# Performance work log

Measured on AMD Instinct MI355X. Metric: run time of the kernel, lower is better.

Reference implementation:

```python
import jax, jax.numpy as jnp
import numpy as np

# SLAYER neuron/simulation constants (netParams)
THETA = 10.0      # spike threshold
TAU_SR = 10.0     # PSP (SRM alpha) time constant
TAU_REF = 1.0     # refractory time constant
TAU_RHO = 1.0     # surrogate-gradient width
SCALE_RHO = 1.0   # surrogate-gradient scale
TS = 1.0          # simulation timestep
K_EPS = 100       # truncated FIR length of the alpha PSP kernel
REF_DECAY = float(np.exp(-TS / TAU_REF))


@jax.custom_vjp
def _spike_fn(v):
    # heaviside threshold with SLAYER-style exponential surrogate gradient
    return (v >= 0.0).astype(v.dtype)

def _spike_fwd(v):
    return (v >= 0.0).astype(v.dtype), v

def _spike_bwd(v, g):
    return (g * (SCALE_RHO / TAU_RHO) * jnp.exp(-jnp.abs(v) / TAU_RHO),)

_spike_fn.defvjp(_spike_fwd, _spike_bwd)


def psp(x):
    """Causal temporal filter with SRM alpha kernel eps(t)=(t/tau)exp(1-t/tau)."""
    shp = x.shape
    T = shp[-1]
    t = jnp.arange(K_EPS, dtype=x.dtype) * TS
    eps = (t / TAU_SR) * jnp.exp(1.0 - t / TAU_SR)
    xr = x.reshape(-1, 1, T)  # [N,1,T]
    y = jax.lax.conv_general_dilated(xr, eps[::-1].reshape(1, 1, K_EPS), (1,), [(K_EPS - 1, 0)])
    return y.reshape(shp)


def spike(u):
    """Sequential threshold with decaying refractory state (scan over time)."""
    uT = jnp.moveaxis(u, -1, 0)  # [T, ...]

    def step(r, u_t):
        s = _spike_fn(u_t + r - THETA)
        return REF_DECAY * r - 2.0 * THETA * s, s

    _, sT = jax.lax.scan(step, jnp.zeros(uT.shape[1:], uT.dtype), uT)
    return jnp.moveaxis(sT, 0, -1)


def pool(x, k):
    # SLAYER pool: fixed-weight sum conv, weight = 1.1*theta/(k*k) per element
    B, C, H, W, T = x.shape
    return x.reshape(B, C, H // k, k, W // k, k, T).sum(axis=(3, 5)) * (1.1 * THETA / (k * k))


def conv(x, w, pad):
    # 3D conv with time-pointwise kernel == per-timestep 2D conv (fold T into batch)
    B, C, H, W, T = x.shape
    xr = jnp.moveaxis(x, -1, 1).reshape(B * T, C, H, W)
    y = jax.lax.conv_general_dilated(xr, w, (1, 1), [(pad, pad), (pad, pad)])
    return jnp.moveaxis(y.reshape(B, T, w.shape[0], H, W), 1, -1)


def delay(x, d):
    """Per-channel learnable temporal delay via linear interpolation gather."""
    T = x.shape[-1]
    C = d.shape[0]
    t = jnp.arange(T, dtype=x.dtype)
    src = t[None, :] - d[:, None]            # [C, T]
    i0 = jnp.floor(src)
    w = (src - i0).reshape((1, C, 1, 1, T))
    i0 = i0.astype(jnp.int32)

    def take(idx):
        v = jnp.take_along_axis(x, jnp.clip(idx, 0, T - 1).reshape((1, C, 1, 1, T)), axis=-1)
        ok = ((idx >= 0) & (idx < T)).reshape((1, C, 1, 1, T))
        return jnp.where(ok, v, 0.0)

    return take(i0) * (1.0 - w) + take(i0 + 1) * w


def setup_inputs() -> dict:
    key = jax.random.key(0)
    ks = jax.random.split(key, 9)
    B, T = 4, 300
    spikeInput = (jax.random.uniform(ks[0], (B, 2, 128, 128, T)) < 0.03).astype(jnp.float32)
    conv1_w = jax.random.normal(ks[1], (16, 2, 5, 5), jnp.float32) * (1.0 / np.sqrt(2 * 25))
    conv2_w = jax.random.normal(ks[2], (32, 16, 3, 3), jnp.float32) * (1.0 / np.sqrt(16 * 9))
    fc1_w = jax.random.normal(ks[3], (512, 2048), jnp.float32) * (1.0 / np.sqrt(2048))
    fc2_w = jax.random.normal(ks[4], (11, 512), jnp.float32) * (1.0 / np.sqrt(512))
    delay1_d = jax.random.uniform(ks[5], (16,), jnp.float32) * 4.0
    delay2_d = jax.random.uniform(ks[6], (32,), jnp.float32) * 4.0
    delay3_d = jax.random.uniform(ks[7], (512,), jnp.float32) * 4.0
    return {"spikeInput": spikeInput, "conv1_w": conv1_w, "conv2_w": conv2_w,
            "fc1_w": fc1_w, "fc2_w": fc2_w,
            "delay1_d": delay1_d, "delay2_d": delay2_d, "delay3_d": delay3_d}


def reference(spikeInput, conv1_w, conv2_w, fc1_w, fc2_w, delay1_d, delay2_d, delay3_d):
    s = spike(pool(psp(spikeInput), 4))          # [B,2,32,32,T]
    s = spike(conv(psp(s), conv1_w, 2))          # [B,16,32,32,T]
    s = delay(s, delay1_d)
    s = spike(pool(psp(s), 2))                   # [B,16,16,16,T]
    s = spike(conv(psp(s), conv2_w, 1))          # [B,32,16,16,T]
    s = delay(s, delay2_d)
    s = spike(pool(psp(s), 2))                   # [B,32,8,8,T]
    B, C, H, W, T = s.shape
    s = s.reshape(B, C * H * W, 1, 1, T)         # [B,2048,1,1,T]
    s = spike(jnp.einsum('oi,bixyt->boxyt', fc1_w, psp(s)))  # [B,512,1,1,T]
    s = delay(s, delay3_d)
    s = spike(jnp.einsum('oi,bixyt->boxyt', fc2_w, psp(s)))  # [B,11,1,1,T]
    return s
```

## Files before the change

kernel.cpp:

```cpp
#include <hip/hip_runtime.h>

#define TLEN 300
#define THETA 10.0f
#define REF_DECAY 0.36787944117144233f

__global__ void eps_init_kernel(float* __restrict__ eps) {
  int k = threadIdx.x;
  if (k < 104) eps[k] = 0.f;
  if (k < 100) {
    float a = (float)k / 10.0f;
    eps[k] = a * expf(1.0f - a);
  }
}

#define FIRSTEP(e, A, B, C)                                                              \
  acc[0] += e.x * B.x; acc[1] += e.x * B.y; acc[2] += e.x * B.z; acc[3] += e.x * B.w;    \
  acc[4] += e.x * C.x; acc[5] += e.x * C.y; acc[6] += e.x * C.z; acc[7] += e.x * C.w;    \
  acc[0] += e.y * A.w; acc[1] += e.y * B.x; acc[2] += e.y * B.y; acc[3] += e.y * B.z;    \
  acc[4] += e.y * B.w; acc[5] += e.y * C.x; acc[6] += e.y * C.y; acc[7] += e.y * C.z;    \
  acc[0] += e.z * A.z; acc[1] += e.z * A.w; acc[2] += e.z * B.x; acc[3] += e.z * B.y;    \
  acc[4] += e.z * B.z; acc[5] += e.z * B.w; acc[6] += e.z * C.x; acc[7] += e.z * C.y;    \
  acc[0] += e.w * A.y; acc[1] += e.w * A.z; acc[2] += e.w * A.w; acc[3] += e.w * B.x;    \
  acc[4] += e.w * B.y; acc[5] += e.w * B.z; acc[6] += e.w * B.w; acc[7] += e.w * C.x;

__device__ __forceinline__ float4 ldq(const float* __restrict__ rowp, int w) {
  if (w >= 0 && w < TLEN) return *reinterpret_cast<const float4*>(rowp + w);
  return make_float4(0.f, 0.f, 0.f, 0.f);
}

__global__ __launch_bounds__(256) void fir_direct_kernel(const float* __restrict__ in,
                                                         float* __restrict__ out,
                                                         const float* __restrict__ epsg,
                                                         int rows) {
  int task = blockIdx.x * 256 + threadIdx.x;
  int row = task / 38;
  int l = task - row * 38;
  if (row >= rows) return;
  const float* rowp = in + (long)row * TLEN;
  const int t0 = 8 * l;
  float4 A = ldq(rowp, t0 - 4);
  float4 B = ldq(rowp, t0);
  float4 C = ldq(rowp, t0 + 4);
  float acc[8];
#pragma unroll
  for (int j = 0; j < 8; ++j) acc[j] = 0.f;
#pragma unroll 1
  for (int kg0 = 0; kg0 < 80; kg0 += 20) {
    const float* ep = epsg + kg0;
#pragma unroll
    for (int kk = 0; kk < 5; ++kk) {
      const float4 e = *reinterpret_cast<const float4*>(ep + 4 * kk);
      const int kg = kg0 + 4 * kk;
      FIRSTEP(e, A, B, C);
      C = B; B = A;
      A = ldq(rowp, t0 - kg - 8);
    }
    __builtin_amdgcn_sched_barrier(0);
  }
#pragma unroll
  for (int kk = 0; kk < 5; ++kk) {
    const float4 e = *reinterpret_cast<const float4*>(epsg + 80 + 4 * kk);
    FIRSTEP(e, A, B, C);
    C = B; B = A;
    if (kk < 4) A = ldq(rowp, t0 - 88 - 4 * kk);
  }
  float* op = out + (long)row * TLEN + t0;
  *reinterpret_cast<float4*>(op) = make_float4(acc[0], acc[1], acc[2], acc[3]);
  if (t0 + 4 < TLEN)
    *reinterpret_cast<float4*>(op + 4) = make_float4(acc[4], acc[5], acc[6], acc[7]);
}

__global__ __launch_bounds__(64) void scan_kernel(float* __restrict__ u, long rows) {
  long row = (long)blockIdx.x * 64 + threadIdx.x;
  if (row >= rows) return;
  float* p = u + row * TLEN;
  float4 q0 = *reinterpret_cast<const float4*>(p);
  float4 q1 = *reinterpret_cast<const float4*>(p + 4);
  float4 q2 = *reinterpret_cast<const float4*>(p + 8);
  float4 q3 = *reinterpret_cast<const float4*>(p + 12);
  float ref = 0.f;
#pragma unroll 4
  for (int c4 = 0; c4 < 75; ++c4) {
    float4 u4 = q0;
    q0 = q1; q1 = q2; q2 = q3;
    if (c4 < 71) q3 = *reinterpret_cast<const float4*>(p + 4 * (c4 + 4));
    float v, sp;
    v = u4.x + ref - THETA; sp = (v >= 0.f) ? 1.f : 0.f; u4.x = sp; ref = REF_DECAY * ref - 20.0f * sp;
    v = u4.y + ref - THETA; sp = (v >= 0.f) ? 1.f : 0.f; u4.y = sp; ref = REF_DECAY * ref - 20.0f * sp;
    v = u4.z + ref - THETA; sp = (v >= 0.f) ? 1.f : 0.f; u4.z = sp; ref = REF_DECAY * ref - 20.0f * sp;
    v = u4.w + ref - THETA; sp = (v >= 0.f) ? 1.f : 0.f; u4.w = sp; ref = REF_DECAY * ref - 20.0f * sp;
    *reinterpret_cast<float4*>(p + 4 * c4) = u4;
  }
}

__global__ __launch_bounds__(64) void scan_reduce4_kernel(const float* __restrict__ part,
                                                          float* __restrict__ s) {
  long row = (long)blockIdx.x * 64 + threadIdx.x;
  const float* p = part + row * TLEN;
  float* o = s + row * TLEN;
  float ref = 0.f;
#pragma unroll 4
  for (int c4 = 0; c4 < 75; ++c4) {
    const float4 v0 = *reinterpret_cast<const float4*>(p + 4 * c4);
    const float4 v1 = *reinterpret_cast<const float4*>(p + 614400 + 4 * c4);
    const float4 v2 = *reinterpret_cast<const float4*>(p + 1228800 + 4 * c4);
    const float4 v3 = *reinterpret_cast<const float4*>(p + 1843200 + 4 * c4);
    float4 u4;
    u4.x = (v0.x + v1.x) + (v2.x + v3.x);
    u4.y = (v0.y + v1.y) + (v2.y + v3.y);
    u4.z = (v0.z + v1.z) + (v2.z + v3.z);
    u4.w = (v0.w + v1.w) + (v2.w + v3.w);
    float v, sp;
    v = u4.x + ref - THETA; sp = (v >= 0.f) ? 1.f : 0.f; u4.x = sp; ref = REF_DECAY * ref - 20.0f * sp;
    v = u4.y + ref - THETA; sp = (v >= 0.f) ? 1.f : 0.f; u4.y = sp; ref = REF_DECAY * ref - 20.0f * sp;
    v = u4.z + ref - THETA; sp = (v >= 0.f) ? 1.f : 0.f; u4.z = sp; ref = REF_DECAY * ref - 20.0f * sp;
    v = u4.w + ref - THETA; sp = (v >= 0.f) ? 1.f : 0.f; u4.w = sp; ref = REF_DECAY * ref - 20.0f * sp;
    *reinterpret_cast<float4*>(o + 4 * c4) = u4;
  }
}

__global__ __launch_bounds__(256) void pool4_kernel(const float* __restrict__ in,
                                                    float* __restrict__ out) {
  int idx = blockIdx.x * 256 + threadIdx.x;
  if (idx >= 153600) return;
  int tq = idx % 75;
  int rest = idx / 75;
  int x = rest & 31; rest >>= 5;
  int y = rest & 31; rest >>= 5;
  const float* base = in + ((long)(rest * 128 + y * 4) * 128 + x * 4) * TLEN + tq * 4;
  float4 s = {0.f, 0.f, 0.f, 0.f};
#pragma unroll
  for (int dy = 0; dy < 4; ++dy)
#pragma unroll
    for (int dx = 0; dx < 4; ++dx) {
      float4 v = *reinterpret_cast<const float4*>(base + (dy * 128 + dx) * TLEN);
      s.x += v.x; s.y += v.y; s.z += v.z; s.w += v.w;
    }
  s.x *= 0.6875f; s.y *= 0.6875f; s.z *= 0.6875f; s.w *= 0.6875f;
  *reinterpret_cast<float4*>(out + ((long)(rest * 32 + y) * 32 + x) * TLEN + tq * 4) = s;
}

__global__ __launch_bounds__(256) void delay_kernel(const float* __restrict__ in,
                                                    const float* __restrict__ d,
                                                    float* __restrict__ out, int total) {
  int idx = blockIdx.x * 256 + threadIdx.x;
  if (idx >= total) return;
  int t = idx % TLEN;
  int rest = idx / TLEN;
  float dd = d[rest & 511];
  float src = (float)t - dd;
  float fi = floorf(src);
  int i0 = (int)fi;
  float wf = src - fi;
  const float* base = in + (long)rest * TLEN;
  float v0 = (i0 >= 0 && i0 < TLEN) ? base[min(max(i0, 0), TLEN - 1)] : 0.f;
  float v1 = (i0 + 1 >= 0 && i0 + 1 < TLEN) ? base[min(max(i0 + 1, 0), TLEN - 1)] : 0.f;
  out[idx] = v0 * (1.f - wf) + v1 * wf;
}

__device__ __forceinline__ int sqz(int r, int q) { return (q & ~7) | ((q + r) & 7); }

__global__ __launch_bounds__(256) void spike_pool2_delay_kernel(const float* __restrict__ u,
                                                                const float* __restrict__ dly,
                                                                float* __restrict__ out,
                                                                int WI, int C) {
  __shared__ float4 ch[64 * 16];
  __shared__ unsigned int bits[64 * 13];
  const int tid = threadIdx.x;
  const long inrow0 = (long)blockIdx.x * 64;
  float ref = 0.f;
  unsigned int wbits = 0;
  for (int cix = 0; cix < 5; ++cix) {
    __syncthreads();
    for (int i = tid; i < 960; i += 256) {
      int r = i / 15, q = i - r * 15;
      ch[r * 16 + sqz(r, q)] = *reinterpret_cast<const float4*>(
          u + (inrow0 + r) * TLEN + cix * 60 + 4 * q);
    }
    __syncthreads();
    if (tid < 64) {
      int r = tid;
#pragma unroll 1
      for (int q = 0; q < 15; ++q) {
        float4 v = ch[r * 16 + sqz(r, q)];
        int t = cix * 60 + 4 * q;
        float x, sp;
        x = v.x + ref - THETA; sp = (x >= 0.f) ? 1.f : 0.f; ref = REF_DECAY * ref - 20.0f * sp;
        wbits |= ((unsigned int)sp) << (t & 31);
        if ((t & 31) == 31) { bits[r * 13 + (t >> 5)] = wbits; wbits = 0; }
        x = v.y + ref - THETA; sp = (x >= 0.f) ? 1.f : 0.f; ref = REF_DECAY * ref - 20.0f * sp;
        wbits |= ((unsigned int)sp) << ((t + 1) & 31);
        if (((t + 1) & 31) == 31) { bits[r * 13 + ((t + 1) >> 5)] = wbits; wbits = 0; }
        x = v.z + ref - THETA; sp = (x >= 0.f) ? 1.f : 0.f; ref = REF_DECAY * ref - 20.0f * sp;
        wbits |= ((unsigned int)sp) << ((t + 2) & 31);
        if (((t + 2) & 31) == 31) { bits[r * 13 + ((t + 2) >> 5)] = wbits; wbits = 0; }
        x = v.w + ref - THETA; sp = (x >= 0.f) ? 1.f : 0.f; ref = REF_DECAY * ref - 20.0f * sp;
        wbits |= ((unsigned int)sp) << ((t + 3) & 31);
        if (((t + 3) & 31) == 31) { bits[r * 13 + ((t + 3) >> 5)] = wbits; wbits = 0; }
      }
    }
  }
  if (tid < 64) bits[tid * 13 + 9] = wbits;
  __syncthreads();
  const int WO = WI >> 1;
  const int bc = (int)(inrow0 / (WI * WI));
  const int y0 = (int)((inrow0 % (WI * WI)) / WI);
  const float dd = dly[bc % C];
  const long orow0 = (long)bc * (WO * WO) + (y0 >> 1) * WO;
  for (int i = tid; i < 4800; i += 256) {
    int ro = i / TLEN, t = i - ro * TLEN;
    int Yr = ro / WO, X = ro - Yr * WO;
    int ir = (2 * Yr) * WI + 2 * X;
    float src = (float)t - dd;
    float fi = floorf(src);
    int i0 = (int)fi;
    float wf = src - fi;
    bool ok0 = (i0 >= 0) && (i0 < TLEN);
    bool ok1 = (i0 + 1 >= 0) && (i0 + 1 < TLEN);
    int j0 = min(max(i0, 0), TLEN - 1);
    int j1 = min(max(i0 + 1, 0), TLEN - 1);
    int s0i = 0, s1i = 0;
#pragma unroll
    for (int dy = 0; dy < 2; ++dy)
#pragma unroll
      for (int dx = 0; dx < 2; ++dx) {
        int rr = ir + dy * WI + dx;
        s0i += (int)((bits[rr * 13 + (j0 >> 5)] >> (j0 & 31)) & 1u);
        s1i += (int)((bits[rr * 13 + (j1 >> 5)] >> (j1 & 31)) & 1u);
      }
    float s0 = ok0 ? (float)s0i : 0.f;
    float s1 = ok1 ? (float)s1i : 0.f;
    out[(orow0 + ro) * TLEN + t] = (s0 * (1.f - wf) + s1 * wf) * 2.75f;
  }
}

__global__ __launch_bounds__(256) void conv1_kernel(const float* __restrict__ in,
                                                    const float* __restrict__ w,
                                                    float* __restrict__ out) {
  __shared__ float xl[11520];
  const int tid = threadIdx.x;
  const int t0 = blockIdx.x * 32;
  const int y = blockIdx.y;
  const int b = blockIdx.z;
  for (int i = tid; i < 2880; i += 256) {
    int tq = i & 7;
    int rest = i >> 3;
    int xp = rest % 36;
    int r2 = rest / 36;
    int dy = r2 % 5;
    int c = r2 / 5;
    int yy = y + dy - 2, xx = xp - 2, t = t0 + tq * 4;
    float4 v = {0.f, 0.f, 0.f, 0.f};
    if (yy >= 0 && yy < 32 && xx >= 0 && xx < 32 && t < TLEN)
      v = *reinterpret_cast<const float4*>(
          in + ((long)((b * 2 + c) * 32 + yy) * 32 + xx) * TLEN + t);
    *reinterpret_cast<float4*>(&xl[rest * 32 + tq * 4]) = v;
  }
  __syncthreads();
  const int tg = tid & 7;
  const int x = tid >> 3;
  float acc[16][4];
#pragma unroll
  for (int o = 0; o < 16; ++o) { acc[o][0] = acc[o][1] = acc[o][2] = acc[o][3] = 0.f; }
  for (int c = 0; c < 2; ++c)
#pragma unroll
    for (int dy = 0; dy < 5; ++dy)
#pragma unroll
      for (int kx = 0; kx < 5; ++kx) {
        const float4 xv = *reinterpret_cast<const float4*>(
            &xl[((c * 5 + dy) * 36 + x + kx) * 32 + tg * 4]);
        const float* wp = w + (c * 5 + dy) * 5 + kx;
#pragma unroll
        for (int o = 0; o < 16; ++o) {
          float wsc = wp[o * 50];
          acc[o][0] += wsc * xv.x; acc[o][1] += wsc * xv.y;
          acc[o][2] += wsc * xv.z; acc[o][3] += wsc * xv.w;
        }
      }
  const int t = t0 + tg * 4;
  if (t < TLEN) {
#pragma unroll
    for (int o = 0; o < 16; ++o) {
      float4 res; res.x = acc[o][0]; res.y = acc[o][1]; res.z = acc[o][2]; res.w = acc[o][3];
      *reinterpret_cast<float4*>(&out[((long)((b * 16 + o) * 32 + y) * 32 + x) * TLEN + t]) = res;
    }
  }
}

__global__ __launch_bounds__(256) void conv2_kernel(const float* __restrict__ in,
                                                    const float* __restrict__ w,
                                                    float* __restrict__ out) {
  __shared__ float xl[13824];
  const int tid = threadIdx.x;
  const int t0 = blockIdx.x * 16;
  const int y = blockIdx.y;
  const int b = blockIdx.z;
  for (int i = tid; i < 3456; i += 256) {
    int tq = i & 3;
    int rest = i >> 2;
    int xp = rest % 18;
    int r2 = rest / 18;
    int dy = r2 % 3;
    int c = r2 / 3;
    int yy = y + dy - 1, xx = xp - 1, t = t0 + tq * 4;
    float4 v = {0.f, 0.f, 0.f, 0.f};
    if (yy >= 0 && yy < 16 && xx >= 0 && xx < 16 && t < TLEN)
      v = *reinterpret_cast<const float4*>(
          in + ((long)((b * 16 + c) * 16 + yy) * 16 + xx) * TLEN + t);
    *reinterpret_cast<float4*>(&xl[rest * 16 + tq * 4]) = v;
  }
  __syncthreads();
  const int tg = tid & 3;
  const int x = (tid >> 2) & 15;
  const int oh = tid >> 6;
  float acc[8][4];
#pragma unroll
  for (int o = 0; o < 8; ++o) { acc[o][0] = acc[o][1] = acc[o][2] = acc[o][3] = 0.f; }
  for (int c = 0; c < 16; ++c)
#pragma unroll
    for (int dy = 0; dy < 3; ++dy)
#pragma unroll
      for (int kx = 0; kx < 3; ++kx) {
        const float4 xv = *reinterpret_cast<const float4*>(
            &xl[((c * 3 + dy) * 18 + x + kx) * 16 + tg * 4]);
        const float* wp = w + (c * 3 + dy) * 3 + kx;
#pragma unroll
        for (int oo = 0; oo < 8; ++oo) {
          float wsc = wp[(oh * 8 + oo) * 144];
          acc[oo][0] += wsc * xv.x; acc[oo][1] += wsc * xv.y;
          acc[oo][2] += wsc * xv.z; acc[oo][3] += wsc * xv.w;
        }
      }
  const int t = t0 + tg * 4;
  if (t < TLEN) {
#pragma unroll
    for (int oo = 0; oo < 8; ++oo) {
      int o = oh * 8 + oo;
      float4 res; res.x = acc[oo][0]; res.y = acc[oo][1]; res.z = acc[oo][2]; res.w = acc[oo][3];
      *reinterpret_cast<float4*>(&out[((long)((b * 32 + o) * 16 + y) * 16 + x) * TLEN + t]) = res;
    }
  }
}

__global__ __launch_bounds__(256) void fc1_kernel(const float* __restrict__ x,
                                                  const float* __restrict__ w,
                                                  float* __restrict__ part) {
  __shared__ float wl[64][44];
  __shared__ float xlb[32][68];
  const int tid = threadIdx.x;
  const int t0 = blockIdx.x * 64;
  const int o0 = blockIdx.y * 64;
  const int b = blockIdx.z >> 2;
  const int split = blockIdx.z & 3;
  const int tx = tid & 15, ty = tid >> 4;
  float acc[4][4];
#pragma unroll
  for (int i = 0; i < 4; ++i)
#pragma unroll
    for (int j = 0; j < 4; ++j) acc[i][j] = 0.f;
  const int kbeg = split * 512;
  for (int kc = kbeg; kc < kbeg + 512; kc += 32) {
    __syncthreads();
#pragma unroll
    for (int rr = 0; rr < 2; ++rr) {
      int i = rr * 256 + tid;
      int ol = i >> 3, kq = i & 7;
      float4 v = *reinterpret_cast<const float4*>(w + (long)(o0 + ol) * 2048 + kc + kq * 4);
      *reinterpret_cast<float4*>(&wl[ol][kq * 4]) = v;
    }
#pragma unroll
    for (int rr = 0; rr < 2; ++rr) {
      int i = rr * 256 + tid;
      int kl = i >> 4, tq = i & 15;
      int t = t0 + tq * 4;
      float4 v = {0.f, 0.f, 0.f, 0.f};
      if (t < TLEN)
        v = *reinterpret_cast<const float4*>(x + ((long)b * 2048 + kc + kl) * TLEN + t);
      *reinterpret_cast<float4*>(&xlb[kl][tq * 4]) = v;
    }
    __syncthreads();
#pragma unroll
    for (int k4 = 0; k4 < 8; ++k4) {
      float4 wq[4], xq[4];
#pragma unroll
      for (int i = 0; i < 4; ++i)
        wq[i] = *reinterpret_cast<const float4*>(&wl[ty * 4 + i][k4 * 4]);
#pragma unroll
      for (int j = 0; j < 4; ++j)
        xq[j] = *reinterpret_cast<const float4*>(&xlb[k4 * 4 + j][tx * 4]);
#pragma unroll
      for (int i = 0; i < 4; ++i) {
        float wa[4] = {wq[i].x, wq[i].y, wq[i].z, wq[i].w};
#pragma unroll
        for (int j = 0; j < 4; ++j) {
          float xa[4] = {xq[j].x, xq[j].y, xq[j].z, xq[j].w};
          acc[i][0] += wa[j] * xa[0]; acc[i][1] += wa[j] * xa[1];
          acc[i][2] += wa[j] * xa[2]; acc[i][3] += wa[j] * xa[3];
        }
      }
    }
  }
  const int t = t0 + tx * 4;
  if (t < TLEN) {
#pragma unroll
    for (int i = 0; i < 4; ++i) {
      float4 res; res.x = acc[i][0]; res.y = acc[i][1]; res.z = acc[i][2]; res.w = acc[i][3];
      *reinterpret_cast<float4*>(
          part + ((long)(split * 4 + b) * 512 + o0 + ty * 4 + i) * TLEN + t) = res;
    }
  }
}

__global__ __launch_bounds__(320) void fc2_spike_kernel(const float* __restrict__ x,
                                                        const float* __restrict__ w,
                                                        float* __restrict__ out) {
  __shared__ float ul[304];
  int blk = blockIdx.x;
  int b = blk / 11, o = blk % 11;
  int t = threadIdx.x;
  if (t < TLEN) {
    const float* xr = x + (long)b * 512 * TLEN + t;
    const float* wr = w + o * 512;
    float a0 = 0.f, a1 = 0.f, a2 = 0.f, a3 = 0.f;
#pragma unroll 4
    for (int i = 0; i < 512; i += 4) {
      a0 += wr[i] * xr[(long)i * TLEN];
      a1 += wr[i + 1] * xr[(long)(i + 1) * TLEN];
      a2 += wr[i + 2] * xr[(long)(i + 2) * TLEN];
      a3 += wr[i + 3] * xr[(long)(i + 3) * TLEN];
    }
    ul[t] = (a0 + a1) + (a2 + a3);
  }
  __syncthreads();
  if (t == 0) {
    float ref = 0.f;
#pragma unroll 4
    for (int c = 0; c < TLEN; ++c) {
      float v = ul[c] + ref - THETA;
      float sp = (v >= 0.f) ? 1.f : 0.f;
      ul[c] = sp;
      ref = REF_DECAY * ref - 20.0f * sp;
    }
  }
  __syncthreads();
  if (t < TLEN) out[((long)b * 11 + o) * TLEN + t] = ul[t];
}

extern "C" void kernel_launch(void* const* d_in, const int* in_sizes, int n_in,
                              void* d_out, int out_size, void* d_ws, size_t ws_size,
                              hipStream_t stream) {
  const float* input = (const float*)d_in[0];
  const float* w1    = (const float*)d_in[1];
  const float* w2    = (const float*)d_in[2];
  const float* wfc1  = (const float*)d_in[3];
  const float* wfc2  = (const float*)d_in[4];
  const float* d1    = (const float*)d_in[5];
  const float* d2    = (const float*)d_in[6];
  const float* d3    = (const float*)d_in[7];

  float* ws   = (float*)d_ws;
  float* big0 = ws;
  float* medA = big0 + 19660800;
  float* medB = medA + 4915200;
  float* fcA  = medB + 4915200;
  float* fcB  = fcA + 614400;
  float* eps  = fcB + 614400;

  hipLaunchKernelGGL(eps_init_kernel, dim3(1), dim3(128), 0, stream, eps);

  hipLaunchKernelGGL(pool4_kernel, dim3(600), dim3(256), 0, stream, input, medA);
  hipLaunchKernelGGL(fir_direct_kernel, dim3(1216), dim3(256), 0, stream, medA, medB, eps, 8192);
  hipLaunchKernelGGL(scan_kernel, dim3(128), dim3(64), 0, stream, medB, 8192L);
  hipLaunchKernelGGL(fir_direct_kernel, dim3(1216), dim3(256), 0, stream, medB, medA, eps, 8192);
  hipLaunchKernelGGL(conv1_kernel, dim3(10, 32, 4), dim3(256), 0, stream, medA, w1, big0);
  hipLaunchKernelGGL(spike_pool2_delay_kernel, dim3(1024), dim3(256), 0, stream,
                     big0, d1, medB, 32, 16);
  hipLaunchKernelGGL(fir_direct_kernel, dim3(2432), dim3(256), 0, stream, medB, medA, eps, 16384);
  hipLaunchKernelGGL(scan_kernel, dim3(256), dim3(64), 0, stream, medA, 16384L);
  hipLaunchKernelGGL(fir_direct_kernel, dim3(2432), dim3(256), 0, stream, medA, medB, eps, 16384);
  hipLaunchKernelGGL(conv2_kernel, dim3(19, 16, 4), dim3(256), 0, stream, medB, w2, big0);
  hipLaunchKernelGGL(spike_pool2_delay_kernel, dim3(512), dim3(256), 0, stream,
                     big0, d2, medA, 16, 32);
  hipLaunchKernelGGL(fir_direct_kernel, dim3(1216), dim3(256), 0, stream, medA, medB, eps, 8192);
  hipLaunchKernelGGL(scan_kernel, dim3(128), dim3(64), 0, stream, medB, 8192L);
  hipLaunchKernelGGL(fir_direct_kernel, dim3(1216), dim3(256), 0, stream, medB, medA, eps, 8192);
  hipLaunchKernelGGL(fc1_kernel, dim3(5, 8, 16), dim3(256), 0, stream, medA, wfc1, big0);
  hipLaunchKernelGGL(scan_reduce4_kernel, dim3(32), dim3(64), 0, stream, big0, fcA);
  hipLaunchKernelGGL(delay_kernel, dim3(2400), dim3(256), 0, stream, fcA, d3, fcB, 614400);
  hipLaunchKernelGGL(fir_direct_kernel, dim3(304), dim3(256), 0, stream, fcB, fcA, eps, 2048);
  hipLaunchKernelGGL(fc2_spike_kernel, dim3(44), dim3(320), 0, stream, fcA, wfc2, (float*)d_out);
}
```

Baseline: 479.0 us.

## Replace FIR PSP with recursive IIR scan fused with spike and delay

Measured after the change: 554.8 us. +15.8%, slower.

```diff
diff --git a/kernel.cpp b/kernel.cpp
--- a/kernel.cpp
+++ b/kernel.cpp
@@ -4,118 +4,121 @@
 #define THETA 10.0f
 #define REF_DECAY 0.36787944117144233f
 
-__global__ void eps_init_kernel(float* __restrict__ eps) {
-  int k = threadIdx.x;
-  if (k < 104) eps[k] = 0.f;
-  if (k < 100) {
-    float a = (float)k / 10.0f;
-    eps[k] = a * expf(1.0f - a);
-  }
-}
-
-#define FIRSTEP(e, A, B, C)                                                              \
-  acc[0] += e.x * B.x; acc[1] += e.x * B.y; acc[2] += e.x * B.z; acc[3] += e.x * B.w;    \
-  acc[4] += e.x * C.x; acc[5] += e.x * C.y; acc[6] += e.x * C.z; acc[7] += e.x * C.w;    \
-  acc[0] += e.y * A.w; acc[1] += e.y * B.x; acc[2] += e.y * B.y; acc[3] += e.y * B.z;    \
-  acc[4] += e.y * B.w; acc[5] += e.y * C.x; acc[6] += e.y * C.y; acc[7] += e.y * C.z;    \
-  acc[0] += e.z * A.z; acc[1] += e.z * A.w; acc[2] += e.z * B.x; acc[3] += e.z * B.y;    \
-  acc[4] += e.z * B.z; acc[5] += e.z * B.w; acc[6] += e.z * C.x; acc[7] += e.z * C.y;    \
-  acc[0] += e.w * A.y; acc[1] += e.w * A.z; acc[2] += e.w * A.w; acc[3] += e.w * B.x;    \
-  acc[4] += e.w * B.y; acc[5] += e.w * B.z; acc[6] += e.w * B.w; acc[7] += e.w * C.x;
-
-__device__ __forceinline__ float4 ldq(const float* __restrict__ rowp, int w) {
-  if (w >= 0 && w < TLEN) return *reinterpret_cast<const float4*>(rowp + w);
-  return make_float4(0.f, 0.f, 0.f, 0.f);
-}
-
-__global__ __launch_bounds__(256) void fir_direct_kernel(const float* __restrict__ in,
-                                                         float* __restrict__ out,
-                                                         const float* __restrict__ epsg,
-                                                         int rows) {
-  int task = blockIdx.x * 256 + threadIdx.x;
-  int row = task / 38;
-  int l = task - row * 38;
+#define R_ 0.9048374180359595732
+#define C_ 0.2718281828459045235
+#define R100_ 4.5399929762484852e-05
+#define CR100_ (C_ * R100_)
+#define C100R100_ (100.0 * C_ * R100_)
+
+__device__ __forceinline__ float psp_step(double& PA, double& QA, double& PB, double& QB,
+                                          double xa, double xb) {
+  QA = R_ * (QA + PA); PA = R_ * PA + xa;
+  QB = R_ * (QB + PB); PB = R_ * PB + xb;
+  return (float)(C_ * QA - CR100_ * QB - C100R100_ * PB);
+}
+
+__device__ __forceinline__ float bit_at(unsigned h0, unsigned h1, unsigned h2, unsigned h3,
+                                        int age) {
+  if (age < 0 || age > 127) return 0.f;
+  unsigned wsel;
+  switch (age >> 5) {
+    case 0: wsel = h0; break;
+    case 1: wsel = h1; break;
+    case 2: wsel = h2; break;
+    default: wsel = h3; break;
+  }
+  return (float)((wsel >> (age & 31)) & 1u);
+}
+
+#define PSPSUB(XA, XB, YO)                                                              \
+  {                                                                                     \
+    float u = psp_step(PA1, QA1, PB1, QB1, (double)(XA), (double)(XB));                 \
+    float v = u + ref - THETA;                                                          \
+    float sp = (v >= 0.f) ? 1.f : 0.f;                                                  \
+    ref = REF_DECAY * ref - 20.0f * sp;                                                 \
+    h3 = (h3 << 1) | (h2 >> 31); h2 = (h2 << 1) | (h1 >> 31);                           \
+    h1 = (h1 << 1) | (h0 >> 31); h0 = (h0 << 1) | (unsigned)sp;                         \
+    YO = psp_step(PA2, QA2, PB2, QB2, (double)sp, (double)((h3 >> 4) & 1u));            \
+  }
+
+__global__ __launch_bounds__(256) void psp_spike_psp_scan_kernel(const float* __restrict__ in,
+                                                                 float* __restrict__ out,
+                                                                 long rows) {
+  long row = (long)blockIdx.x * 256 + threadIdx.x;
   if (row >= rows) return;
-  const float* rowp = in + (long)row * TLEN;
-  const int t0 = 8 * l;
-  float4 A = ldq(rowp, t0 - 4);
-  float4 B = ldq(rowp, t0);
-  float4 C = ldq(rowp, t0 + 4);
-  float acc[8];
-#pragma unroll
-  for (int j = 0; j < 8; ++j) acc[j] = 0.f;
+  const float* xr = in + row * TLEN;
+  float* yr = out + row * TLEN;
+  double PA1 = 0, QA1 = 0, PB1 = 0, QB1 = 0;
+  double PA2 = 0, QA2 = 0, PB2 = 0, QB2 = 0;
+  float ref = 0.f;
+  unsigned h0 = 0, h1 = 0, h2 = 0, h3 = 0;
 #pragma unroll 1
-  for (int kg0 = 0; kg0 < 80; kg0 += 20) {
-    const float* ep = epsg + kg0;
-#pragma unroll
-    for (int kk = 0; kk < 5; ++kk) {
-      const float4 e = *reinterpret_cast<const float4*>(ep + 4 * kk);
-      const int kg = kg0 + 4 * kk;
-      FIRSTEP(e, A, B, C);
-      C = B; B = A;
-      A = ldq(rowp, t0 - kg - 8);
-    }
-    __builtin_amdgcn_sched_barrier(0);
-  }
-#pragma unroll
-  for (int kk = 0; kk < 5; ++kk) {
-    const float4 e = *reinterpret_cast<const float4*>(epsg + 80 + 4 * kk);
-    FIRSTEP(e, A, B, C);
-    C = B; B = A;
-    if (kk < 4) A = ldq(rowp, t0 - 88 - 4 * kk);
-  }
-  float* op = out + (long)row * TLEN + t0;
-  *reinterpret_cast<float4*>(op) = make_float4(acc[0], acc[1], acc[2], acc[3]);
-  if (t0 + 4 < TLEN)
-    *reinterpret_cast<float4*>(op + 4) = make_float4(acc[4], acc[5], acc[6], acc[7]);
-}
-
-__global__ __launch_bounds__(64) void scan_kernel(float* __restrict__ u, long rows) {
-  long row = (long)blockIdx.x * 64 + threadIdx.x;
-  if (row >= rows) return;
-  float* p = u + row * TLEN;
-  float4 q0 = *reinterpret_cast<const float4*>(p);
-  float4 q1 = *reinterpret_cast<const float4*>(p + 4);
-  float4 q2 = *reinterpret_cast<const float4*>(p + 8);
-  float4 q3 = *reinterpret_cast<const float4*>(p + 12);
+  for (int tq = 0; tq < 75; ++tq) {
+    const int t = 4 * tq;
+    const float4 xa = *reinterpret_cast<const float4*>(xr + t);
+    float4 xb = make_float4(0.f, 0.f, 0.f, 0.f);
+    if (t >= 100) xb = *reinterpret_cast<const float4*>(xr + t - 100);
+    float4 yo;
+    PSPSUB(xa.x, xb.x, yo.x);
+    PSPSUB(xa.y, xb.y, yo.y);
+    PSPSUB(xa.z, xb.z, yo.z);
+    PSPSUB(xa.w, xb.w, yo.w);
+    *reinterpret_cast<float4*>(yr + t) = yo;
+  }
+}
+
+#define RSDPSUB(C0, C1, C2, C3, TT, YO)                                                 \
+  {                                                                                     \
+    const int t = (TT);                                                                 \
+    float u = ((C0) + (C1)) + ((C2) + (C3));                                            \
+    float v = u + ref - THETA;                                                          \
+    float sp = (v >= 0.f) ? 1.f : 0.f;                                                  \
+    ref = REF_DECAY * ref - 20.0f * sp;                                                 \
+    h3 = (h3 << 1) | (h2 >> 31); h2 = (h2 << 1) | (h1 >> 31);                           \
+    h1 = (h1 << 1) | (h0 >> 31); h0 = (h0 << 1) | (unsigned)sp;                         \
+    float src = (float)t - dd;                                                          \
+    float fi = floorf(src);                                                             \
+    int i0 = (int)fi;                                                                   \
+    float w = src - fi;                                                                 \
+    float s0 = bit_at(h0, h1, h2, h3, t - i0);                                          \
+    float s1 = bit_at(h0, h1, h2, h3, t - i0 - 1);                                      \
+    float z = s0 * (1.f - w) + s1 * w;                                                  \
+    float zb = 0.f;                                                                     \
+    if (t >= 100) {                                                                     \
+      float src2 = (float)(t - 100) - dd;                                               \
+      float fi2 = floorf(src2);                                                         \
+      int i02 = (int)fi2;                                                               \
+      float w2 = src2 - fi2;                                                            \
+      float s0b = bit_at(h0, h1, h2, h3, t - i02);                                      \
+      float s1b = bit_at(h0, h1, h2, h3, t - i02 - 1);                                  \
+      zb = s0b * (1.f - w2) + s1b * w2;                                                 \
+    }                                                                                   \
+    YO = psp_step(PA, QA, PB, QB, (double)z, (double)zb);                               \
+  }
+
+__global__ __launch_bounds__(256) void reduce_spike_delay_psp_scan_kernel(
+    const float* __restrict__ part, const float* __restrict__ dly,
+    float* __restrict__ out) {
+  long row = (long)blockIdx.x * 256 + threadIdx.x;
+  const float* p = part + row * TLEN;
+  float* yr = out + row * TLEN;
+  const float dd = dly[(int)(row & 511)];
+  double PA = 0, QA = 0, PB = 0, QB = 0;
   float ref = 0.f;
-#pragma unroll 4
-  for (int c4 = 0; c4 < 75; ++c4) {
-    float4 u4 = q0;
-    q0 = q1; q1 = q2; q2 = q3;
-    if (c4 < 71) q3 = *reinterpret_cast<const float4*>(p + 4 * (c4 + 4));
-    float v, sp;
-    v = u4.x + ref - THETA; sp = (v >= 0.f) ? 1.f : 0.f; u4.x = sp; ref = REF_DECAY * ref - 20.0f * sp;
-    v = u4.y + ref - THETA; sp = (v >= 0.f) ? 1.f : 0.f; u4.y = sp; ref = REF_DECAY * ref - 20.0f * sp;
-    v = u4.z + ref - THETA; sp = (v >= 0.f) ? 1.f : 0.f; u4.z = sp; ref = REF_DECAY * ref - 20.0f * sp;
-    v = u4.w + ref - THETA; sp = (v >= 0.f) ? 1.f : 0.f; u4.w = sp; ref = REF_DECAY * ref - 20.0f * sp;
-    *reinterpret_cast<float4*>(p + 4 * c4) = u4;
-  }
-}
-
-__global__ __launch_bounds__(64) void scan_reduce4_kernel(const float* __restrict__ part,
-                                                          float* __restrict__ s) {
-  long row = (long)blockIdx.x * 64 + threadIdx.x;
-  const float* p = part + row * TLEN;
-  float* o = s + row * TLEN;
-  float ref = 0.f;
-#pragma unroll 4
-  for (int c4 = 0; c4 < 75; ++c4) {
-    const float4 v0 = *reinterpret_cast<const float4*>(p + 4 * c4);
-    const float4 v1 = *reinterpret_cast<const float4*>(p + 614400 + 4 * c4);
-    const float4 v2 = *reinterpret_cast<const float4*>(p + 1228800 + 4 * c4);
-    const float4 v3 = *reinterpret_cast<const float4*>(p + 1843200 + 4 * c4);
-    float4 u4;
-    u4.x = (v0.x + v1.x) + (v2.x + v3.x);
-    u4.y = (v0.y + v1.y) + (v2.y + v3.y);
-    u4.z = (v0.z + v1.z) + (v2.z + v3.z);
-    u4.w = (v0.w + v1.w) + (v2.w + v3.w);
-    float v, sp;
-    v = u4.x + ref - THETA; sp = (v >= 0.f) ? 1.f : 0.f; u4.x = sp; ref = REF_DECAY * ref - 20.0f * sp;
-    v = u4.y + ref - THETA; sp = (v >= 0.f) ? 1.f : 0.f; u4.y = sp; ref = REF_DECAY * ref - 20.0f * sp;
-    v = u4.z + ref - THETA; sp = (v >= 0.f) ? 1.f : 0.f; u4.z = sp; ref = REF_DECAY * ref - 20.0f * sp;
-    v = u4.w + ref - THETA; sp = (v >= 0.f) ? 1.f : 0.f; u4.w = sp; ref = REF_DECAY * ref - 20.0f * sp;
-    *reinterpret_cast<float4*>(o + 4 * c4) = u4;
+  unsigned h0 = 0, h1 = 0, h2 = 0, h3 = 0;
+#pragma unroll 1
+  for (int tq = 0; tq < 75; ++tq) {
+    const int t4 = 4 * tq;
+    const float4 v0 = *reinterpret_cast<const float4*>(p + t4);
+    const float4 v1 = *reinterpret_cast<const float4*>(p + 614400 + t4);
+    const float4 v2 = *reinterpret_cast<const float4*>(p + 1228800 + t4);
+    const float4 v3 = *reinterpret_cast<const float4*>(p + 1843200 + t4);
+    float4 yo;
+    RSDPSUB(v0.x, v1.x, v2.x, v3.x, t4 + 0, yo.x);
+    RSDPSUB(v0.y, v1.y, v2.y, v3.y, t4 + 1, yo.y);
+    RSDPSUB(v0.z, v1.z, v2.z, v3.z, t4 + 2, yo.z);
+    RSDPSUB(v0.w, v1.w, v2.w, v3.w, t4 + 3, yo.w);
+    *reinterpret_cast<float4*>(yr + t4) = yo;
   }
 }
 
@@ -138,24 +141,6 @@
     }
   s.x *= 0.6875f; s.y *= 0.6875f; s.z *= 0.6875f; s.w *= 0.6875f;
   *reinterpret_cast<float4*>(out + ((long)(rest * 32 + y) * 32 + x) * TLEN + tq * 4) = s;
-}
-
-__global__ __launch_bounds__(256) void delay_kernel(const float* __restrict__ in,
-                                                    const float* __restrict__ d,
-                                                    float* __restrict__ out, int total) {
-  int idx = blockIdx.x * 256 + threadIdx.x;
-  if (idx >= total) return;
-  int t = idx % TLEN;
-  int rest = idx / TLEN;
-  float dd = d[rest & 511];
-  float src = (float)t - dd;
-  float fi = floorf(src);
-  int i0 = (int)fi;
-  float wf = src - fi;
-  const float* base = in + (long)rest * TLEN;
-  float v0 = (i0 >= 0 && i0 < TLEN) ? base[min(max(i0, 0), TLEN - 1)] : 0.f;
-  float v1 = (i0 + 1 >= 0 && i0 + 1 < TLEN) ? base[min(max(i0 + 1, 0), TLEN - 1)] : 0.f;
-  out[idx] = v0 * (1.f - wf) + v1 * wf;
 }
 
 __device__ __forceinline__ int sqz(int r, int q) { return (q & ~7) | ((q + r) & 7); }
@@ -464,29 +449,22 @@
   float* medB = medA + 4915200;
   float* fcA  = medB + 4915200;
   float* fcB  = fcA + 614400;
-  float* eps  = fcB + 614400;
-
-  hipLaunchKernelGGL(eps_init_kernel, dim3(1), dim3(128), 0, stream, eps);
 
   hipLaunchKernelGGL(pool4_kernel, dim3(600), dim3(256), 0, stream, input, medA);
-  hipLaunchKernelGGL(fir_direct_kernel, dim3(1216), dim3(256), 0, stream, medA, medB, eps, 8192);
-  hipLaunchKernelGGL(scan_kernel, dim3(128), dim3(64), 0, stream, medB, 8192L);
-  hipLaunchKernelGGL(fir_direct_kernel, dim3(1216), dim3(256), 0, stream, medB, medA, eps, 8192);
-  hipLaunchKernelGGL(conv1_kernel, dim3(10, 32, 4), dim3(256), 0, stream, medA, w1, big0);
+  hipLaunchKernelGGL(psp_spike_psp_scan_kernel, dim3(32), dim3(256), 0, stream,
+                     medA, medB, 8192L);
+  hipLaunchKernelGGL(conv1_kernel, dim3(10, 32, 4), dim3(256), 0, stream, medB, w1, big0);
   hipLaunchKernelGGL(spike_pool2_delay_kernel, dim3(1024), dim3(256), 0, stream,
-                     big0, d1, medB, 32, 16);
-  hipLaunchKernelGGL(fir_direct_kernel, dim3(2432), dim3(256), 0, stream, medB, medA, eps, 16384);
-  hipLaunchKernelGGL(scan_kernel, dim3(256), dim3(64), 0, stream, medA, 16384L);
-  hipLaunchKernelGGL(fir_direct_kernel, dim3(2432), dim3(256), 0, stream, medA, medB, eps, 16384);
+                     big0, d1, medA, 32, 16);
+  hipLaunchKernelGGL(psp_spike_psp_scan_kernel, dim3(64), dim3(256), 0, stream,
+                     medA, medB, 16384L);
   hipLaunchKernelGGL(conv2_kernel, dim3(19, 16, 4), dim3(256), 0, stream, medB, w2, big0);
   hipLaunchKernelGGL(spike_pool2_delay_kernel, dim3(512), dim3(256), 0, stream,
                      big0, d2, medA, 16, 32);
-  hipLaunchKernelGGL(fir_direct_kernel, dim3(1216), dim3(256), 0, stream, medA, medB, eps, 8192);
-  hipLaunchKernelGGL(scan_kernel, dim3(128), dim3(64), 0, stream, medB, 8192L);
-  hipLaunchKernelGGL(fir_direct_kernel, dim3(1216), dim3(256), 0, stream, medB, medA, eps, 8192);
-  hipLaunchKernelGGL(fc1_kernel, dim3(5, 8, 16), dim3(256), 0, stream, medA, wfc1, big0);
-  hipLaunchKernelGGL(scan_reduce4_kernel, dim3(32), dim3(64), 0, stream, big0, fcA);
-  hipLaunchKernelGGL(delay_kernel, dim3(2400), dim3(256), 0, stream, fcA, d3, fcB, 614400);
-  hipLaunchKernelGGL(fir_direct_kernel, dim3(304), dim3(256), 0, stream, fcB, fcA, eps, 2048);
-  hipLaunchKernelGGL(fc2_spike_kernel, dim3(44), dim3(320), 0, stream, fcA, wfc2, (float*)d_out);
-}
+  hipLaunchKernelGGL(psp_spike_psp_scan_kernel, dim3(32), dim3(256), 0, stream,
+                     medA, medB, 8192L);
+  hipLaunchKernelGGL(fc1_kernel, dim3(5, 8, 16), dim3(256), 0, stream, medB, wfc1, big0);
+  hipLaunchKernelGGL(reduce_spike_delay_psp_scan_kernel, dim3(8), dim3(256), 0, stream,
+                     big0, d3, fcB);
+  hipLaunchKernelGGL(fc2_spike_kernel, dim3(44), dim3(320), 0, stream, fcB, wfc2, (float*)d_out);
+}
```

## Replace FIR-scan-FIR chains with fused recursive IIR psp-spike-psp scan kernel

Applied to the files above, without the earlier changes.

Result: faster. 443.0 us (median of 2 runs) (-7.5%).

```diff
diff --git a/kernel.cpp b/kernel.cpp
--- a/kernel.cpp
+++ b/kernel.cpp
@@ -3,6 +3,13 @@
 #define TLEN 300
 #define THETA 10.0f
 #define REF_DECAY 0.36787944117144233f
+
+#define R_ 0.9048374180359595732
+#define C_ 0.2718281828459045235
+#define R100_ 4.5399929762484852e-05
+#define RF_ ((float)R_)
+#define CR100F_ ((float)(C_ * R100_))
+#define C100R100F_ ((float)(100.0 * C_ * R100_))
 
 __global__ void eps_init_kernel(float* __restrict__ eps) {
   int k = threadIdx.x;
@@ -11,6 +18,69 @@
     float a = (float)k / 10.0f;
     eps[k] = a * expf(1.0f - a);
   }
+}
+
+#define PSPSUB(XA, XB, YO)                                                              \
+  {                                                                                     \
+    QA1 = R_ * (QA1 + PA1); PA1 = R_ * PA1 + (double)(XA);                              \
+    QB1 = RF_ * (QB1 + PB1); PB1 = RF_ * PB1 + (XB);                                    \
+    float u = (float)(C_ * QA1) - (CR100F_ * QB1 + C100R100F_ * PB1);                   \
+    float v = u + ref - THETA;                                                          \
+    float sp = (v >= 0.f) ? 1.f : 0.f;                                                  \
+    ref = REF_DECAY * ref - 20.0f * sp;                                                 \
+    h3 = (h3 << 1) | (h2 >> 31); h2 = (h2 << 1) | (h1 >> 31);                           \
+    h1 = (h1 << 1) | (h0 >> 31); h0 = (h0 << 1) | (unsigned)sp;                         \
+    float spb = (float)((h3 >> 4) & 1u);                                                \
+    QA2 = R_ * (QA2 + PA2); PA2 = R_ * PA2 + (double)sp;                                \
+    QB2 = RF_ * (QB2 + PB2); PB2 = RF_ * PB2 + spb;                                     \
+    YO = (float)(C_ * QA2) - (CR100F_ * QB2 + C100R100F_ * PB2);                        \
+  }
+
+__global__ __launch_bounds__(64) void psp_spike_psp_scan_kernel(const float* __restrict__ in,
+                                                                float* __restrict__ out,
+                                                                long rows) {
+  long row = (long)blockIdx.x * 64 + threadIdx.x;
+  if (row >= rows) return;
+  const float* xr = in + row * TLEN;
+  float* yr = out + row * TLEN;
+  double PA1 = 0, QA1 = 0, PA2 = 0, QA2 = 0;
+  float PB1 = 0.f, QB1 = 0.f, PB2 = 0.f, QB2 = 0.f;
+  float ref = 0.f;
+  unsigned h0 = 0, h1 = 0, h2 = 0, h3 = 0;
+#pragma unroll 1
+  for (int tq = 0; tq < 75; ++tq) {
+    const int t = 4 * tq;
+    const float4 xa = *reinterpret_cast<const float4*>(xr + t);
+    float4 xb = make_float4(0.f, 0.f, 0.f, 0.f);
+    if (t >= 100) xb = *reinterpret_cast<const float4*>(xr + t - 100);
+    float4 yo;
+    PSPSUB(xa.x, xb.x, yo.x);
+    PSPSUB(xa.y, xb.y, yo.y);
+    PSPSUB(xa.z, xb.z, yo.z);
+    PSPSUB(xa.w, xb.w, yo.w);
+    *reinterpret_cast<float4*>(yr + t) = yo;
+  }
+}
+
+__global__ __launch_bounds__(256) void pool4_kernel(const float* __restrict__ in,
+                                                    float* __restrict__ out) {
+  int idx = blockIdx.x * 256 + threadIdx.x;
+  if (idx >= 153600) return;
+  int tq = idx % 75;
+  int rest = idx / 75;
+  int x = rest & 31; rest >>= 5;
+  int y = rest & 31; rest >>= 5;
+  const float* base = in + ((long)(rest * 128 + y * 4) * 128 + x * 4) * TLEN + tq * 4;
+  float4 s = {0.f, 0.f, 0.f, 0.f};
+#pragma unroll
+  for (int dy = 0; dy < 4; ++dy)
+#pragma unroll
+    for (int dx = 0; dx < 4; ++dx) {
+      float4 v = *reinterpret_cast<const float4*>(base + (dy * 128 + dx) * TLEN);
+      s.x += v.x; s.y += v.y; s.z += v.z; s.w += v.w;
+    }
+  s.x *= 0.6875f; s.y *= 0.6875f; s.z *= 0.6875f; s.w *= 0.6875f;
+  *reinterpret_cast<float4*>(out + ((long)(rest * 32 + y) * 32 + x) * TLEN + tq * 4) = s;
 }
 
 #define FIRSTEP(e, A, B, C)                                                              \
@@ -68,29 +138,6 @@
   *reinterpret_cast<float4*>(op) = make_float4(acc[0], acc[1], acc[2], acc[3]);
   if (t0 + 4 < TLEN)
     *reinterpret_cast<float4*>(op + 4) = make_float4(acc[4], acc[5], acc[6], acc[7]);
-}
-
-__global__ __launch_bounds__(64) void scan_kernel(float* __restrict__ u, long rows) {
-  long row = (long)blockIdx.x * 64 + threadIdx.x;
-  if (row >= rows) return;
-  float* p = u + row * TLEN;
-  float4 q0 = *reinterpret_cast<const float4*>(p);
-  float4 q1 = *reinterpret_cast<const float4*>(p + 4);
-  float4 q2 = *reinterpret_cast<const float4*>(p + 8);
-  float4 q3 = *reinterpret_cast<const float4*>(p + 12);
-  float ref = 0.f;
-#pragma unroll 4
-  for (int c4 = 0; c4 < 75; ++c4) {
-    float4 u4 = q0;
-    q0 = q1; q1 = q2; q2 = q3;
-    if (c4 < 71) q3 = *reinterpret_cast<const float4*>(p + 4 * (c4 + 4));
-    float v, sp;
-    v = u4.x + ref - THETA; sp = (v >= 0.f) ? 1.f : 0.f; u4.x = sp; ref = REF_DECAY * ref - 20.0f * sp;
-    v = u4.y + ref - THETA; sp = (v >= 0.f) ? 1.f : 0.f; u4.y = sp; ref = REF_DECAY * ref - 20.0f * sp;
-    v = u4.z + ref - THETA; sp = (v >= 0.f) ? 1.f : 0.f; u4.z = sp; ref = REF_DECAY * ref - 20.0f * sp;
-    v = u4.w + ref - THETA; sp = (v >= 0.f) ? 1.f : 0.f; u4.w = sp; ref = REF_DECAY * ref - 20.0f * sp;
-    *reinterpret_cast<float4*>(p + 4 * c4) = u4;
-  }
 }
 
 __global__ __launch_bounds__(64) void scan_reduce4_kernel(const float* __restrict__ part,
@@ -119,27 +166,6 @@
   }
 }
 
-__global__ __launch_bounds__(256) void pool4_kernel(const float* __restrict__ in,
-                                                    float* __restrict__ out) {
-  int idx = blockIdx.x * 256 + threadIdx.x;
-  if (idx >= 153600) return;
-  int tq = idx % 75;
-  int rest = idx / 75;
-  int x = rest & 31; rest >>= 5;
-  int y = rest & 31; rest >>= 5;
-  const float* base = in + ((long)(rest * 128 + y * 4) * 128 + x * 4) * TLEN + tq * 4;
-  float4 s = {0.f, 0.f, 0.f, 0.f};
-#pragma unroll
-  for (int dy = 0; dy < 4; ++dy)
-#pragma unroll
-    for (int dx = 0; dx < 4; ++dx) {
-      float4 v = *reinterpret_cast<const float4*>(base + (dy * 128 + dx) * TLEN);
-      s.x += v.x; s.y += v.y; s.z += v.z; s.w += v.w;
-    }
-  s.x *= 0.6875f; s.y *= 0.6875f; s.z *= 0.6875f; s.w *= 0.6875f;
-  *reinterpret_cast<float4*>(out + ((long)(rest * 32 + y) * 32 + x) * TLEN + tq * 4) = s;
-}
-
 __global__ __launch_bounds__(256) void delay_kernel(const float* __restrict__ in,
                                                     const float* __restrict__ d,
                                                     float* __restrict__ out, int total) {
@@ -469,22 +495,19 @@
   hipLaunchKernelGGL(eps_init_kernel, dim3(1), dim3(128), 0, stream, eps);
 
   hipLaunchKernelGGL(pool4_kernel, dim3(600), dim3(256), 0, stream, input, medA);
-  hipLaunchKernelGGL(fir_direct_kernel, dim3(1216), dim3(256), 0, stream, medA, medB, eps, 8192);
-  hipLaunchKernelGGL(scan_kernel, dim3(128), dim3(64), 0, stream, medB, 8192L);
-  hipLaunchKernelGGL(fir_direct_kernel, dim3(1216), dim3(256), 0, stream, medB, medA, eps, 8192);
-  hipLaunchKernelGGL(conv1_kernel, dim3(10, 32, 4), dim3(256), 0, stream, medA, w1, big0);
+  hipLaunchKernelGGL(psp_spike_psp_scan_kernel, dim3(128), dim3(64), 0, stream,
+                     medA, medB, 8192L);
+  hipLaunchKernelGGL(conv1_kernel, dim3(10, 32, 4), dim3(256), 0, stream, medB, w1, big0);
   hipLaunchKernelGGL(spike_pool2_delay_kernel, dim3(1024), dim3(256), 0, stream,
-                     big0, d1, medB, 32, 16);
-  hipLaunchKernelGGL(fir_direct_kernel, dim3(2432), dim3(256), 0, stream, medB, medA, eps, 16384);
-  hipLaunchKernelGGL(scan_kernel, dim3(256), dim3(64), 0, stream, medA, 16384L);
-  hipLaunchKernelGGL(fir_direct_kernel, dim3(2432), dim3(256), 0, stream, medA, medB, eps, 16384);
+                     big0, d1, medA, 32, 16);
+  hipLaunchKernelGGL(psp_spike_psp_scan_kernel, dim3(256), dim3(64), 0, stream,
+                     medA, medB, 16384L);
   hipLaunchKernelGGL(conv2_kernel, dim3(19, 16, 4), dim3(256), 0, stream, medB, w2, big0);
   hipLaunchKernelGGL(spike_pool2_delay_kernel, dim3(512), dim3(256), 0, stream,
                      big0, d2, medA, 16, 32);
-  hipLaunchKernelGGL(fir_direct_kernel, dim3(1216), dim3(256), 0, stream, medA, medB, eps, 8192);
-  hipLaunchKernelGGL(scan_kernel, dim3(128), dim3(64), 0, stream, medB, 8192L);
-  hipLaunchKernelGGL(fir_direct_kernel, dim3(1216), dim3(256), 0, stream, medB, medA, eps, 8192);
-  hipLaunchKernelGGL(fc1_kernel, dim3(5, 8, 16), dim3(256), 0, stream, medA, wfc1, big0);
+  hipLaunchKernelGGL(psp_spike_psp_scan_kernel, dim3(128), dim3(64), 0, stream,
+                     medA, medB, 8192L);
+  hipLaunchKernelGGL(fc1_kernel, dim3(5, 8, 16), dim3(256), 0, stream, medB, wfc1, big0);
   hipLaunchKernelGGL(scan_reduce4_kernel, dim3(32), dim3(64), 0, stream, big0, fcA);
   hipLaunchKernelGGL(delay_kernel, dim3(2400), dim3(256), 0, stream, fcA, d3, fcB, 614400);
   hipLaunchKernelGGL(fir_direct_kernel, dim3(304), dim3(256), 0, stream, fcB, fcA, eps, 2048);
```
